# Optimization experiments

Hardware: AMD Instinct MI355X
Metric: run time of the kernel (lower is better)

The kernel has to match this reference:

```python
import jax, jax.numpy as jnp
import numpy as np

ALPHA = 0.2  # LeakyReLU negative slope
MASK_VAL = -9e15


def setup_inputs() -> dict:
    key = jax.random.key(0)
    k1, k2, k3 = jax.random.split(key, 3)
    bs, N, d = 16, 1024, 128
    h = jax.random.normal(k1, (bs, N, d), dtype=jnp.float32)
    # nn.Linear(in, out, bias=False).weight has shape [out, in]
    W = jax.random.normal(k2, (d, d), dtype=jnp.float32) * (1.414 / np.sqrt(d))
    # a: Linear(2*out, 1) -> weight [1, 2d] flattened to [2d], bias [1]
    a_w = jax.random.normal(k3, (2 * d,), dtype=jnp.float32) * 0.1
    a_b = jnp.zeros((1,), dtype=jnp.float32)
    return {"h": h, "W": W, "a_w": a_w, "a_b": a_b}


def reference(h, W, a_w, a_b):
    # h: [bs, N, d], W: [d, d] (torch Linear weight), a_w: [2d], a_b: [1]
    bs, N, d = h.shape
    Wh = jnp.einsum('bnd,fd->bnf', h, W)  # [bs, N, d]
    # Decompose a([Wh_i ; Wh_j]) = Wh_i . a1 + Wh_j . a2 + b  (avoids O(N^2 * 2d) concat)
    a1, a2 = a_w[:d], a_w[d:]
    s1 = Wh @ a1  # [bs, N] -- source-node contribution (row index i)
    s2 = Wh @ a2  # [bs, N] -- target-node contribution (col index j)
    e = jax.nn.leaky_relu(s1[:, :, None] + s2[:, None, :] + a_b[0], negative_slope=ALPHA)
    # adj = ones - eye: mask out the diagonal (self-edges)
    diag = jnp.eye(N, dtype=bool)
    e = jnp.where(diag[None, :, :], MASK_VAL, e)
    attention = jax.nn.softmax(e, axis=-1)  # [bs, N, N]
    h_prime = jnp.einsum('bij,bjf->bif', attention, Wh)
    return jax.nn.elu(h_prime)  # concat=True applies ELU
```

## Files before the change

kernel.cpp:

```cpp
#include <hip/hip_runtime.h>
#include <hip/hip_bf16.h>
#include <stdint.h>

#define LOG2E 1.4426950408889634f

typedef float f32x4 __attribute__((ext_vector_type(4)));
typedef short s16x8 __attribute__((ext_vector_type(8)));
typedef int   i32x4 __attribute__((ext_vector_type(4)));

__device__ __forceinline__ float bf2f(uint16_t u) {
    uint32_t x = ((uint32_t)u) << 16;
    float f;
    __builtin_memcpy(&f, &x, 4);
    return f;
}
__device__ __forceinline__ uint16_t f2bf(float f) {
    uint32_t x;
    __builtin_memcpy(&x, &f, 4);
    uint32_t r = (x + 0x7fffu + ((x >> 16) & 1u)) >> 16;
    return (uint16_t)r;
}

__global__ __launch_bounds__(256) void k0_splitW(
    const float* __restrict__ W, uint16_t* __restrict__ whi, uint16_t* __restrict__ wlo)
{
    int i = blockIdx.x * 256 + threadIdx.x;
    float x = W[i];
    uint16_t hb = f2bf(x);
    whi[i] = hb;
    wlo[i] = f2bf(x - bf2f(hb));
}

__global__ __launch_bounds__(256) void k1_gemm(
    const float* __restrict__ h, const uint16_t* __restrict__ whi_,
    const uint16_t* __restrict__ wlo_,
    const float* __restrict__ aw, const float* __restrict__ ab,
    uint16_t* __restrict__ whB, float* __restrict__ s1b, float* __restrict__ s2g,
    float* __restrict__ smaxrg)
{
    __shared__ float sred[4][16][2];
    const int tid = threadIdx.x;
    const int w = tid >> 6, lane = tid & 63;
    const int q = lane >> 4, n16 = lane & 15;
    const int R0 = blockIdx.x * 16;
    const int f0 = w * 32;

    f32x4 acc[2];
    acc[0] = 0.f; acc[1] = 0.f;

    const float* hrow = h + (size_t)(R0 + n16) * 128 + q * 8;
    const uint16_t* whbase = whi_ + (size_t)(f0 + n16) * 128 + q * 8;
    const uint16_t* wlbase = wlo_ + (size_t)(f0 + n16) * 128 + q * 8;
#pragma unroll
    for (int kc = 0; kc < 4; ++kc) {
        float4 x0 = *(const float4*)(hrow + kc * 32);
        float4 x1 = *(const float4*)(hrow + kc * 32 + 4);
        float xs[8] = {x0.x, x0.y, x0.z, x0.w, x1.x, x1.y, x1.z, x1.w};
        s16x8 ahi, alo;
#pragma unroll
        for (int t = 0; t < 8; ++t) {
            uint16_t hb = f2bf(xs[t]);
            ahi[t] = (short)hb;
            alo[t] = (short)f2bf(xs[t] - bf2f(hb));
        }
#pragma unroll
        for (int fb = 0; fb < 2; ++fb) {
            s16x8 bhi = *(const s16x8*)(whbase + fb * 16 * 128 + kc * 32);
            s16x8 blo = *(const s16x8*)(wlbase + fb * 16 * 128 + kc * 32);
            acc[fb] = __builtin_amdgcn_mfma_f32_16x16x32_bf16(ahi, bhi, acc[fb], 0, 0, 0);
            acc[fb] = __builtin_amdgcn_mfma_f32_16x16x32_bf16(alo, bhi, acc[fb], 0, 0, 0);
            acc[fb] = __builtin_amdgcn_mfma_f32_16x16x32_bf16(ahi, blo, acc[fb], 0, 0, 0);
        }
    }

    float s1p[4] = {0.f, 0.f, 0.f, 0.f}, s2p[4] = {0.f, 0.f, 0.f, 0.f};
#pragma unroll
    for (int fb = 0; fb < 2; ++fb) {
        float a1 = aw[f0 + fb * 16 + n16];
        float a2 = aw[128 + f0 + fb * 16 + n16];
#pragma unroll
        for (int reg = 0; reg < 4; ++reg) {
            s1p[reg] = fmaf(acc[fb][reg], a1, s1p[reg]);
            s2p[reg] = fmaf(acc[fb][reg], a2, s2p[reg]);
        }
    }
#pragma unroll
    for (int off = 1; off < 16; off <<= 1) {
#pragma unroll
        for (int reg = 0; reg < 4; ++reg) {
            s1p[reg] += __shfl_xor(s1p[reg], off);
            s2p[reg] += __shfl_xor(s2p[reg], off);
        }
    }
    if (n16 == 0) {
#pragma unroll
        for (int reg = 0; reg < 4; ++reg) {
            sred[w][q * 4 + reg][0] = s1p[reg];
            sred[w][q * 4 + reg][1] = s2p[reg];
        }
    }
    __syncthreads();
    if (tid < 16) {
        float s1 = sred[0][tid][0] + sred[1][tid][0] + sred[2][tid][0] + sred[3][tid][0];
        float s2 = sred[0][tid][1] + sred[1][tid][1] + sred[2][tid][1] + sred[3][tid][1];
        int R = R0 + tid;
        s1b[R] = LOG2E * (s1 + ab[0]);
        float s2s = LOG2E * s2;
        s2g[R] = s2s;
        float m = s2s;
#pragma unroll
        for (int off = 1; off < 16; off <<= 1)
            m = fmaxf(m, __shfl_xor(m, off));
        if (tid == 0) smaxrg[blockIdx.x] = m;
    }

    const int b = R0 >> 10;
    const int jt = (R0 & 1023) >> 5;
    const int rg1 = (R0 >> 4) & 1;
    uint16_t* base = whB + (size_t)b * 131072 + (size_t)jt * 512;
    const int lane8p = (rg1 * 2 + (q >> 1)) * 16 + n16;
#pragma unroll
    for (int fb = 0; fb < 2; ++fb) {
        int fblk = w * 2 + fb;
        uint32_t e0 = f2bf(acc[fb][0]), e1 = f2bf(acc[fb][1]);
        uint32_t e2 = f2bf(acc[fb][2]), e3 = f2bf(acc[fb][3]);
        uint2 val = make_uint2(e0 | (e1 << 16), e2 | (e3 << 16));
        *(uint2*)(base + fblk * 16384 + lane8p * 8 + (q & 1) * 4) = val;
    }
}

__global__ __launch_bounds__(64) void k2_attn(
    const uint16_t* __restrict__ whB, const float* __restrict__ s1b,
    const float* __restrict__ s2g, const float* __restrict__ smaxrg,
    float* __restrict__ out)
{
    const int lane = threadIdx.x;
    const int q = lane >> 4, n16 = lane & 15;
    const int idx = blockIdx.x;
    const int xcd = idx & 7;
    const int o = idx >> 3;
    const int b = ((o >> 7) << 3) | xcd;
    const int rem = o & 127;
    const int rg = rem >> 2;
    const int fq = rem & 3;
    const int jb = b << 10;
    const int iw0 = rg * 32;
    const int f0 = fq * 32;

    float M = smaxrg[(b << 6) | lane];
#pragma unroll
    for (int off = 1; off < 64; off <<= 1)
        M = fmaxf(M, __shfl_xor(M, off));

    float Ai[2], Bi[2];
#pragma unroll
    for (int rf = 0; rf < 2; ++rf) {
        float s1v = s1b[jb + iw0 + rf * 16 + n16];
        float tm = s1v + M;
        float mi = fmaxf(tm, 0.2f * tm);
        Ai[rf] = s1v - mi;
        Bi[rf] = fmaf(0.2f, s1v, -mi);
    }

    f32x4 acc[2][2], accl[2];
#pragma unroll
    for (int rf = 0; rf < 2; ++rf) {
        acc[rf][0] = 0.f; acc[rf][1] = 0.f; accl[rf] = 0.f;
    }

    s16x8 Bones;
#pragma unroll
    for (int t = 0; t < 8; ++t) Bones[t] = (short)0x3F80;

    const uint16_t* wb = whB + ((size_t)b << 17) + lane * 8;
    const float* ug = s2g + jb + q * 8;
    const int fblk0 = fq * 2, fblk1 = fq * 2 + 1;

    s16x8 Bc0 = *(const s16x8*)(wb + fblk0 * 16384);
    s16x8 Bc1 = *(const s16x8*)(wb + fblk1 * 16384);

    for (int jt = 0; jt < 32; ++jt) {
        const int jn = (jt < 31) ? jt + 1 : 31;
        const uint16_t* bpn = wb + jn * 512;
        s16x8 Bn0 = *(const s16x8*)(bpn + fblk0 * 16384);
        s16x8 Bn1 = *(const s16x8*)(bpn + fblk1 * 16384);

        float4 ua = *(const float4*)(ug + jt * 32);
        float4 ub = *(const float4*)(ug + jt * 32 + 4);
        float uv[8] = {ua.x, ua.y, ua.z, ua.w, ub.x, ub.y, ub.z, ub.w};

        s16x8 A[2];
#pragma unroll
        for (int rf = 0; rf < 2; ++rf) {
            i32x4 pk;
#pragma unroll
            for (int pr = 0; pr < 4; ++pr) {
                float p0 = __builtin_amdgcn_exp2f(
                    fmaxf(Ai[rf] + uv[2 * pr], fmaf(0.2f, uv[2 * pr], Bi[rf])));
                float p1 = __builtin_amdgcn_exp2f(
                    fmaxf(Ai[rf] + uv[2 * pr + 1], fmaf(0.2f, uv[2 * pr + 1], Bi[rf])));
                pk[pr] = (int)((__builtin_bit_cast(uint32_t, p0) >> 16) |
                               (__builtin_bit_cast(uint32_t, p1) & 0xffff0000u));
            }
            A[rf] = __builtin_bit_cast(s16x8, pk);
        }
#pragma unroll
        for (int rf = 0; rf < 2; ++rf) {
            acc[rf][0] = __builtin_amdgcn_mfma_f32_16x16x32_bf16(A[rf], Bc0, acc[rf][0], 0, 0, 0);
            acc[rf][1] = __builtin_amdgcn_mfma_f32_16x16x32_bf16(A[rf], Bc1, acc[rf][1], 0, 0, 0);
            accl[rf]   = __builtin_amdgcn_mfma_f32_16x16x32_bf16(A[rf], Bones, accl[rf], 0, 0, 0);
        }
        Bc0 = Bn0; Bc1 = Bn1;
    }

#pragma unroll
    for (int rf = 0; rf < 2; ++rf) {
#pragma unroll
        for (int reg = 0; reg < 4; ++reg) {
            int iw = iw0 + rf * 16 + q * 4 + reg;
            float s1v = s1b[jb + iw];
            float tm = s1v + M;
            float mi = fmaxf(tm, 0.2f * tm);
            float u_i = s2g[jb + iw];
            float arg = fmaxf((s1v - mi) + u_i, fmaf(0.2f, u_i, fmaf(0.2f, s1v, -mi)));
            float p = __builtin_amdgcn_exp2f(arg);
            float pt = __builtin_bit_cast(float, __builtin_bit_cast(uint32_t, p) & 0xffff0000u);
            accl[rf][reg] -= pt;
            int lane_i = ((iw >> 3) & 3) * 16 + n16;
#pragma unroll
            for (int fb = 0; fb < 2; ++fb) {
                size_t a = ((size_t)b << 17) + (size_t)(fq * 2 + fb) * 16384 +
                           (size_t)(iw >> 5) * 512 + lane_i * 8 + (iw & 7);
                float wv = bf2f(whB[a]);
                acc[rf][fb][reg] -= pt * wv;
            }
        }
    }

#pragma unroll
    for (int rf = 0; rf < 2; ++rf) {
#pragma unroll
        for (int reg = 0; reg < 4; ++reg) {
            float rl = 1.0f / accl[rf][reg];
            int row = jb + iw0 + rf * 16 + q * 4 + reg;
#pragma unroll
            for (int fb = 0; fb < 2; ++fb) {
                float v = acc[rf][fb][reg] * rl;
                float e = v > 0.f ? v : (__builtin_amdgcn_exp2f(v * LOG2E) - 1.f);
                out[(size_t)row * 128 + f0 + fb * 16 + n16] = e;
            }
        }
    }
}

extern "C" void kernel_launch(void* const* d_in, const int* in_sizes, int n_in,
                              void* d_out, int out_size, void* d_ws, size_t ws_size,
                              hipStream_t stream) {
    (void)in_sizes; (void)n_in; (void)out_size; (void)ws_size;
    const float* h  = (const float*)d_in[0];
    const float* W  = (const float*)d_in[1];
    const float* aw = (const float*)d_in[2];
    const float* ab = (const float*)d_in[3];
    float* out = (float*)d_out;

    uint16_t* whB = (uint16_t*)d_ws;
    float* s1b    = (float*)((char*)d_ws + (4u << 20));
    float* s2g    = s1b + 16384;
    float* smaxrg = s2g + 16384;
    uint16_t* whi = (uint16_t*)(smaxrg + 1024);
    uint16_t* wlo = whi + 16384;

    k0_splitW<<<64, 256, 0, stream>>>(W, whi, wlo);
    k1_gemm<<<1024, 256, 0, stream>>>(h, whi, wlo, aw, ab, whB, s1b, s2g, smaxrg);
    k2_attn<<<2048, 64, 0, stream>>>(whB, s1b, s2g, smaxrg, out);
}
```

Before: 100.8 us.

## Factor exp of leaky-relu score into precomputed per-node exponentials

The per-element exp2 in the attention inner loop is replaced by a product of precomputed exponentials. Since exp2 is monotonic, exp2(max(a+u, b+0.2u)) equals max(exp2(a)*exp2(u), exp2(b)*exp2(0.2u)). The GEMM kernel now writes exp2(s2) and exp2(0.2*s2) per node, and the attention kernel computes two multiplies and a max per element, packing to bf16 with a byte permute. This removes transcendental work from the hot loop but doubles the per-column score loads, which are now prefetched one tile ahead, and it adds some risk of overflow or underflow in the separated exponentials.

```diff
diff --git a/kernel.cpp b/kernel.cpp
--- a/kernel.cpp
+++ b/kernel.cpp
@@ -35,7 +35,8 @@
     const float* __restrict__ h, const uint16_t* __restrict__ whi_,
     const uint16_t* __restrict__ wlo_,
     const float* __restrict__ aw, const float* __restrict__ ab,
-    uint16_t* __restrict__ whB, float* __restrict__ s1b, float* __restrict__ s2g,
+    uint16_t* __restrict__ whB, float* __restrict__ s1b,
+    float* __restrict__ E1g, float* __restrict__ E2g,
     float* __restrict__ smaxrg)
 {
     __shared__ float sred[4][16][2];
@@ -106,7 +107,8 @@
         int R = R0 + tid;
         s1b[R] = LOG2E * (s1 + ab[0]);
         float s2s = LOG2E * s2;
-        s2g[R] = s2s;
+        E1g[R] = __builtin_amdgcn_exp2f(s2s);
+        E2g[R] = __builtin_amdgcn_exp2f(0.2f * s2s);
         float m = s2s;
 #pragma unroll
         for (int off = 1; off < 16; off <<= 1)
@@ -131,8 +133,8 @@
 
 __global__ __launch_bounds__(64) void k2_attn(
     const uint16_t* __restrict__ whB, const float* __restrict__ s1b,
-    const float* __restrict__ s2g, const float* __restrict__ smaxrg,
-    float* __restrict__ out)
+    const float* __restrict__ E1g, const float* __restrict__ E2g,
+    const float* __restrict__ smaxrg, float* __restrict__ out)
 {
     const int lane = threadIdx.x;
     const int q = lane >> 4, n16 = lane & 15;
@@ -152,14 +154,14 @@
     for (int off = 1; off < 64; off <<= 1)
         M = fmaxf(M, __shfl_xor(M, off));
 
-    float Ai[2], Bi[2];
+    float eA[2], eB[2];
 #pragma unroll
     for (int rf = 0; rf < 2; ++rf) {
         float s1v = s1b[jb + iw0 + rf * 16 + n16];
         float tm = s1v + M;
         float mi = fmaxf(tm, 0.2f * tm);
-        Ai[rf] = s1v - mi;
-        Bi[rf] = fmaf(0.2f, s1v, -mi);
+        eA[rf] = __builtin_amdgcn_exp2f(s1v - mi);
+        eB[rf] = __builtin_amdgcn_exp2f(fmaf(0.2f, s1v, -mi));
     }
 
     f32x4 acc[2][2], accl[2];
@@ -173,21 +175,29 @@
     for (int t = 0; t < 8; ++t) Bones[t] = (short)0x3F80;
 
     const uint16_t* wb = whB + ((size_t)b << 17) + lane * 8;
-    const float* ug = s2g + jb + q * 8;
+    const float* e1p = E1g + jb + q * 8;
+    const float* e2p = E2g + jb + q * 8;
     const int fblk0 = fq * 2, fblk1 = fq * 2 + 1;
 
     s16x8 Bc0 = *(const s16x8*)(wb + fblk0 * 16384);
     s16x8 Bc1 = *(const s16x8*)(wb + fblk1 * 16384);
+    float4 c1a = *(const float4*)(e1p);
+    float4 c1b = *(const float4*)(e1p + 4);
+    float4 c2a = *(const float4*)(e2p);
+    float4 c2b = *(const float4*)(e2p + 4);
 
     for (int jt = 0; jt < 32; ++jt) {
         const int jn = (jt < 31) ? jt + 1 : 31;
         const uint16_t* bpn = wb + jn * 512;
         s16x8 Bn0 = *(const s16x8*)(bpn + fblk0 * 16384);
         s16x8 Bn1 = *(const s16x8*)(bpn + fblk1 * 16384);
-
-        float4 ua = *(const float4*)(ug + jt * 32);
-        float4 ub = *(const float4*)(ug + jt * 32 + 4);
-        float uv[8] = {ua.x, ua.y, ua.z, ua.w, ub.x, ub.y, ub.z, ub.w};
+        float4 n1a = *(const float4*)(e1p + jn * 32);
+        float4 n1b = *(const float4*)(e1p + jn * 32 + 4);
+        float4 n2a = *(const float4*)(e2p + jn * 32);
+        float4 n2b = *(const float4*)(e2p + jn * 32 + 4);
+
+        float e1v[8] = {c1a.x, c1a.y, c1a.z, c1a.w, c1b.x, c1b.y, c1b.z, c1b.w};
+        float e2v[8] = {c2a.x, c2a.y, c2a.z, c2a.w, c2b.x, c2b.y, c2b.z, c2b.w};
 
         s16x8 A[2];
 #pragma unroll
@@ -195,12 +205,11 @@
             i32x4 pk;
 #pragma unroll
             for (int pr = 0; pr < 4; ++pr) {
-                float p0 = __builtin_amdgcn_exp2f(
-                    fmaxf(Ai[rf] + uv[2 * pr], fmaf(0.2f, uv[2 * pr], Bi[rf])));
-                float p1 = __builtin_amdgcn_exp2f(
-                    fmaxf(Ai[rf] + uv[2 * pr + 1], fmaf(0.2f, uv[2 * pr + 1], Bi[rf])));
-                pk[pr] = (int)((__builtin_bit_cast(uint32_t, p0) >> 16) |
-                               (__builtin_bit_cast(uint32_t, p1) & 0xffff0000u));
+                float p0 = fmaxf(eA[rf] * e1v[2 * pr],     eB[rf] * e2v[2 * pr]);
+                float p1 = fmaxf(eA[rf] * e1v[2 * pr + 1], eB[rf] * e2v[2 * pr + 1]);
+                pk[pr] = (int)__builtin_amdgcn_perm(
+                    __builtin_bit_cast(uint32_t, p1),
+                    __builtin_bit_cast(uint32_t, p0), 0x07060302u);
             }
             A[rf] = __builtin_bit_cast(s16x8, pk);
         }
@@ -211,6 +220,7 @@
             accl[rf]   = __builtin_amdgcn_mfma_f32_16x16x32_bf16(A[rf], Bones, accl[rf], 0, 0, 0);
         }
         Bc0 = Bn0; Bc1 = Bn1;
+        c1a = n1a; c1b = n1b; c2a = n2a; c2b = n2b;
     }
 
 #pragma unroll
@@ -221,9 +231,9 @@
             float s1v = s1b[jb + iw];
             float tm = s1v + M;
             float mi = fmaxf(tm, 0.2f * tm);
-            float u_i = s2g[jb + iw];
-            float arg = fmaxf((s1v - mi) + u_i, fmaf(0.2f, u_i, fmaf(0.2f, s1v, -mi)));
-            float p = __builtin_amdgcn_exp2f(arg);
+            float eAr = __builtin_amdgcn_exp2f(s1v - mi);
+            float eBr = __builtin_amdgcn_exp2f(fmaf(0.2f, s1v, -mi));
+            float p = fmaxf(eAr * E1g[jb + iw], eBr * E2g[jb + iw]);
             float pt = __builtin_bit_cast(float, __builtin_bit_cast(uint32_t, p) & 0xffff0000u);
             accl[rf][reg] -= pt;
             int lane_i = ((iw >> 3) & 3) * 16 + n16;
@@ -265,12 +275,13 @@
 
     uint16_t* whB = (uint16_t*)d_ws;
     float* s1b    = (float*)((char*)d_ws + (4u << 20));
-    float* s2g    = s1b + 16384;
-    float* smaxrg = s2g + 16384;
+    float* E1g    = s1b + 16384;
+    float* E2g    = E1g + 16384;
+    float* smaxrg = E2g + 16384;
     uint16_t* whi = (uint16_t*)(smaxrg + 1024);
     uint16_t* wlo = whi + 16384;
 
     k0_splitW<<<64, 256, 0, stream>>>(W, whi, wlo);
-    k1_gemm<<<1024, 256, 0, stream>>>(h, whi, wlo, aw, ab, whB, s1b, s2g, smaxrg);
-    k2_attn<<<2048, 64, 0, stream>>>(whB, s1b, s2g, smaxrg, out);
-}
+    k1_gemm<<<1024, 256, 0, stream>>>(h, whi, wlo, aw, ab, whB, s1b, E1g, E2g, smaxrg);
+    k2_attn<<<2048, 64, 0, stream>>>(whB, s1b, E1g, E2g, smaxrg, out);
+}
```

New measurement: 94.60 us. 6.1% less time.
